# Kernel tuning notes

Hardware: AMD Instinct MI355X
Metric: run time of the kernel (lower is better)

Reference implementation:

```python
import jax, jax.numpy as jnp
import numpy as np

KERNEL_MUL = 2.0
KERNEL_NUM = 5
EPS = 1e-06


def setup_inputs() -> dict:
    key = jax.random.key(0)
    k1, k2 = jax.random.split(key)
    N, D = 4096, 256
    source = jax.random.normal(k1, (N, D), dtype=jnp.float32)
    target = jax.random.normal(k2, (N, D), dtype=jnp.float32)
    return {"source": source, "target": target}


def reference(source, target):
    n_src = source.shape[0]
    total = jnp.concatenate([source, target], axis=0)  # [2N, D]
    n = total.shape[0]
    # the broadcasted (total0 - total1)**2 sum, without the O(N^2*D) tensor).
    sq = jnp.sum(total * total, axis=1)  # [2N]
    L2 = sq[:, None] + sq[None, :] - 2.0 * (total @ total.T)  # [2N, 2N]
    # Bandwidth from detached distances (torch uses L2_distance.data).
    bandwidth = jax.lax.stop_gradient(jnp.sum(L2)) / (n * n - n)
    bandwidth = bandwidth / (KERNEL_MUL ** (KERNEL_NUM // 2))
    kernels = jnp.zeros_like(L2)
    for i in range(KERNEL_NUM):
        bw = bandwidth * (KERNEL_MUL ** i)
        kernels = kernels + jnp.exp(-L2 / (bw + EPS))
    XX = kernels[:n_src, :n_src]
    YY = kernels[n_src:, n_src:]
    XY = kernels[:n_src, n_src:]
    YX = kernels[n_src:, :n_src]
    return jnp.mean(XX + YY - XY - YX)
```

## Files before the change

### kernel.cpp

```cpp
#include <hip/hip_runtime.h>

#define N_TOT 8192
#define NS 4096
#define D 256
#define NB 64
#define NTRI (NB*(NB+1)/2)
#define HALF_B 32

typedef float f32x16 __attribute__((ext_vector_type(16)));
typedef float f32x2 __attribute__((ext_vector_type(2)));
typedef int i32x4 __attribute__((ext_vector_type(4)));
typedef int i32x8 __attribute__((ext_vector_type(8)));

__device__ __forceinline__ void gload16(const void* g, void* l) {
  __builtin_amdgcn_global_load_lds(
      (const __attribute__((address_space(1))) unsigned int*)g,
      (__attribute__((address_space(3))) unsigned int*)l,
      16, 0, 0);
}

__global__ void k_prep(const float* __restrict__ src, const float* __restrict__ tgt,
                       unsigned char* __restrict__ Xb, float* __restrict__ sqv,
                       float* __restrict__ pm, float* __restrict__ wsqp) {
  __shared__ float colacc[256];
  __shared__ float wred[4];
  int t = threadIdx.x, l = t & 63, w = t >> 6;
  colacc[t] = 0.f;
  __syncthreads();
  int base = blockIdx.x * 32;
  float c0 = 0.f, c1 = 0.f, c2 = 0.f, c3 = 0.f;
  float wsq = 0.f;
  #pragma unroll
  for (int r = 0; r < 8; ++r) {
    int row = base + w * 8 + r;
    const float* p = (row < NS) ? (src + (size_t)row * D) : (tgt + (size_t)(row - NS) * D);
    float4 v = ((const float4*)p)[l];
    int pk = __builtin_amdgcn_cvt_pk_fp8_f32(v.x, v.y, 0, false);
    pk = __builtin_amdgcn_cvt_pk_fp8_f32(v.z, v.w, pk, true);
    ((int*)(Xb + (size_t)row * D))[l] = pk;
    c0 += v.x; c1 += v.y; c2 += v.z; c3 += v.w;
    float s = fmaf(v.x, v.x, fmaf(v.y, v.y, fmaf(v.z, v.z, v.w * v.w)));
    for (int o = 32; o > 0; o >>= 1) s += __shfl_down(s, o, 64);
    if (l == 0) { sqv[row] = s; wsq += s; }
  }
  atomicAdd(&colacc[4 * l + 0], c0);
  atomicAdd(&colacc[4 * l + 1], c1);
  atomicAdd(&colacc[4 * l + 2], c2);
  atomicAdd(&colacc[4 * l + 3], c3);
  if (l == 0) wred[w] = wsq;
  __syncthreads();
  pm[blockIdx.x * 256 + t] = colacc[t];
  if (t == 0) wsqp[blockIdx.x] = (wred[0] + wred[1]) + (wred[2] + wred[3]);
}

__global__ void k_bw(const float* __restrict__ pm, const float* __restrict__ wsqp,
                     float* __restrict__ coef) {
  __shared__ double red[256];
  int t = threadIdx.x;
  float cs = 0.f;
  for (int b = 0; b < 256; ++b) cs += pm[b * 256 + t];
  red[t] = (double)cs * (double)cs;
  __syncthreads();
  for (int s = 128; s > 0; s >>= 1) {
    if (t < s) red[t] += red[t + s];
    __syncthreads();
  }
  double msq = red[0];
  __syncthreads();
  red[t] = (double)wsqp[t];
  __syncthreads();
  for (int s = 128; s > 0; s >>= 1) {
    if (t < s) red[t] += red[t + s];
    __syncthreads();
  }
  if (t == 0) {
    double Sv = red[0];
    double n = (double)N_TOT;
    double sumL2 = 2.0 * n * Sv - 2.0 * msq;
    double bw = sumL2 / (n * n - n) / 4.0;
    double c4 = 1.0 / (bw * 16.0 + 1e-6);
    coef[0] = (float)(c4 * 1.4426950408889634);
  }
}

__global__ __launch_bounds__(256) void k_main(
    const unsigned char* __restrict__ Xb, const float* __restrict__ sqv,
    const float* __restrict__ coef, float* __restrict__ bpart) {
  int b = blockIdx.x;
  int bi = (int)((2.f * NB + 1.f - sqrtf((float)((2 * NB + 1) * (2 * NB + 1) - 8 * b))) * 0.5f);
  if (bi < 0) bi = 0;
  if (bi > NB - 1) bi = NB - 1;
  while ((bi + 1) * (2 * NB - bi) / 2 <= b) ++bi;
  while (bi * (2 * NB - bi + 1) / 2 > b) --bi;
  int bj = bi + (b - bi * (2 * NB - bi + 1) / 2);

  __shared__ __align__(16) unsigned char ldsA[4 * 128 * 64];
  __shared__ __align__(16) unsigned char ldsB[4 * 128 * 64];
  __shared__ float sqA[128], sqB[128];
  __shared__ float redw[4];

  int t = threadIdx.x, l = t & 63, w = t >> 6;
  int lr = l & 31, half = l >> 5;
  int waveRow = w >> 1, waveCol = w & 1;

  const unsigned char* arow = Xb + (size_t)bi * 128 * D;
  const unsigned char* brow = Xb + (size_t)bj * 128 * D;

  #pragma unroll
  for (int p = 0; p < 2; ++p) {
    int seg = p * 256 + t;
    int row = seg >> 2;
    int kb = (seg & 3) ^ (row & 3) ^ ((row >> 2) & 3);
    int gbase = row * D + kb * 16;
    int dbase = (p * 256 + w * 64) * 16;
    #pragma unroll
    for (int ko = 0; ko < 4; ++ko) {
      gload16(arow + gbase + ko * 64, &ldsA[ko * 8192 + dbase]);
      gload16(brow + gbase + ko * 64, &ldsB[ko * 8192 + dbase]);
    }
  }
  if (t < 128) sqA[t] = sqv[bi * 128 + t];
  else         sqB[t - 128] = sqv[bj * 128 + (t - 128)];
  float A4 = coef[0];
  __syncthreads();

  f32x16 acc[2][2] = {};
  int cLo = 2 * half, cHi = 2 * half + 1;

  #pragma unroll
  for (int ko = 0; ko < 4; ++ko) {
    const unsigned char* lA = &ldsA[ko * 8192];
    const unsigned char* lB = &ldsB[ko * 8192];
    i32x8 aF[2];
    #pragma unroll
    for (int rb = 0; rb < 2; ++rb) {
      int rowA = waveRow * 64 + rb * 32 + lr;
      int sw = (rowA & 3) ^ ((rowA >> 2) & 3);
      i32x4 lo = *(const i32x4*)&lA[rowA * 64 + (cLo ^ sw) * 16];
      i32x4 hi = *(const i32x4*)&lA[rowA * 64 + (cHi ^ sw) * 16];
      aF[rb] = (i32x8){lo.x, lo.y, lo.z, lo.w, hi.x, hi.y, hi.z, hi.w};
    }
    #pragma unroll
    for (int cb = 0; cb < 2; ++cb) {
      int rowB = waveCol * 64 + cb * 32 + lr;
      int sw = (rowB & 3) ^ ((rowB >> 2) & 3);
      i32x4 lo = *(const i32x4*)&lB[rowB * 64 + (cLo ^ sw) * 16];
      i32x4 hi = *(const i32x4*)&lB[rowB * 64 + (cHi ^ sw) * 16];
      i32x8 bF = (i32x8){lo.x, lo.y, lo.z, lo.w, hi.x, hi.y, hi.z, hi.w};
      #pragma unroll
      for (int rb = 0; rb < 2; ++rb)
        acc[rb][cb] = __builtin_amdgcn_mfma_scale_f32_32x32x64_f8f6f4(
            aF[rb], bF, acc[rb][cb], 0, 0, 0, 127, 0, 127);
    }
  }

  float c2A4 = 2.f * A4, nA4 = -A4;
  f32x2 lsum2 = {0.f, 0.f};
  bool diag = (bi == bj);
  #pragma unroll
  for (int cb = 0; cb < 2; ++cb) {
    int jj = waveCol * 64 + cb * 32 + lr;
    float bjv = nA4 * sqB[jj];
    #pragma unroll
    for (int rb = 0; rb < 2; ++rb) {
      #pragma unroll
      for (int r = 0; r < 16; r += 2) {
        int ii = waveRow * 64 + rb * 32 + (r & 3) + 8 * (r >> 2) + 4 * half;
        f32x2 dot2 = {acc[rb][cb][r], acc[rb][cb][r + 1]};
        f32x2 sq2 = {sqA[ii], sqA[ii + 1]};
        f32x2 tt = c2A4 * dot2 + (nA4 * sq2 + bjv);
        f32x2 e;
        e.x = __builtin_amdgcn_exp2f(tt.x);
        e.y = __builtin_amdgcn_exp2f(tt.y);
        f32x2 e2 = e * e, e4 = e2 * e2, e8 = e4 * e4, e16 = e8 * e8;
        f32x2 kern = ((e + e2) + (e4 + e8)) + e16;
        if (diag) {
          if (ii == jj) kern.x = 0.f;
          if (ii + 1 == jj) kern.y = 0.f;
        }
        lsum2 += kern;
      }
    }
  }
  float lsum = lsum2.x + lsum2.y;
  for (int o = 32; o > 0; o >>= 1) lsum += __shfl_down(lsum, o, 64);
  if (l == 0) redw[w] = lsum;
  __syncthreads();
  if (t == 0) {
    float tot = (redw[0] + redw[1]) + (redw[2] + redw[3]);
    float wgt = diag ? 1.f : 2.f;
    float sgn = ((bi < HALF_B) == (bj < HALF_B)) ? 1.f : -1.f;
    bpart[b] = tot * wgt * sgn;
  }
}

__global__ void k_final(const float* __restrict__ bpart, float* __restrict__ out) {
  __shared__ double red[256];
  int t = threadIdx.x;
  double s = 0.0;
  for (int k = 0; k < 9; ++k) {
    int idx = k * 256 + t;
    if (idx < NTRI) s += (double)bpart[idx];
  }
  red[t] = s;
  __syncthreads();
  for (int st = 128; st > 0; st >>= 1) {
    if (t < st) red[t] += red[t + st];
    __syncthreads();
  }
  if (t == 0) {
    double total = red[0] + 5.0 * (double)N_TOT;
    out[0] = (float)(total / ((double)NS * (double)NS));
  }
}

extern "C" void kernel_launch(void* const* d_in, const int* in_sizes, int n_in,
                              void* d_out, int out_size, void* d_ws, size_t ws_size,
                              hipStream_t stream) {
  const float* src = (const float*)d_in[0];
  const float* tgt = (const float*)d_in[1];
  float* out = (float*)d_out;
  char* ws = (char*)d_ws;
  unsigned char* Xb = (unsigned char*)ws;
  float* sqv  = (float*)(ws + (4u << 20));
  float* pm   = (float*)(ws + (4u << 20) + (32u << 10));
  float* wsqp = (float*)(ws + (4u << 20) + (288u << 10));
  float* coef = (float*)(ws + (4u << 20) + (289u << 10));
  float* bpart = (float*)(ws + (4u << 20) + (290u << 10));

  hipLaunchKernelGGL(k_prep, dim3(256), dim3(256), 0, stream, src, tgt, Xb, sqv, pm, wsqp);
  hipLaunchKernelGGL(k_bw, dim3(1), dim3(256), 0, stream, pm, wsqp, coef);
  hipLaunchKernelGGL(k_main, dim3(NTRI), dim3(256), 0, stream, Xb, sqv, coef, bpart);
  hipLaunchKernelGGL(k_final, dim3(1), dim3(256), 0, stream, bpart, out);
}
```

Baseline: 98.45 us.

## Process two triangle tiles per block with double-buffered K-chunk pipelining

```diff
diff --git a/kernel.cpp b/kernel.cpp
--- a/kernel.cpp
+++ b/kernel.cpp
@@ -86,51 +86,68 @@
 __global__ __launch_bounds__(256) void k_main(
     const unsigned char* __restrict__ Xb, const float* __restrict__ sqv,
     const float* __restrict__ coef, float* __restrict__ bpart) {
-  int b = blockIdx.x;
-  int bi = (int)((2.f * NB + 1.f - sqrtf((float)((2 * NB + 1) * (2 * NB + 1) - 8 * b))) * 0.5f);
-  if (bi < 0) bi = 0;
-  if (bi > NB - 1) bi = NB - 1;
-  while ((bi + 1) * (2 * NB - bi) / 2 <= b) ++bi;
-  while (bi * (2 * NB - bi + 1) / 2 > b) --bi;
-  int bj = bi + (b - bi * (2 * NB - bi + 1) / 2);
-
-  __shared__ __align__(16) unsigned char ldsA[4 * 128 * 64];
-  __shared__ __align__(16) unsigned char ldsB[4 * 128 * 64];
-  __shared__ float sqA[128], sqB[128];
+  int b0 = blockIdx.x * 2;
+  int bi0 = (int)((2.f * NB + 1.f - sqrtf((float)((2 * NB + 1) * (2 * NB + 1) - 8 * b0))) * 0.5f);
+  if (bi0 < 0) bi0 = 0;
+  if (bi0 > NB - 1) bi0 = NB - 1;
+  while ((bi0 + 1) * (2 * NB - bi0) / 2 <= b0) ++bi0;
+  while (bi0 * (2 * NB - bi0 + 1) / 2 > b0) --bi0;
+  int bj0 = bi0 + (b0 - bi0 * (2 * NB - bi0 + 1) / 2);
+  int bi_[2], bj_[2];
+  bi_[0] = bi0; bj_[0] = bj0;
+  bool wrap = (bj0 + 1 > NB - 1);
+  bi_[1] = wrap ? bi0 + 1 : bi0;
+  bj_[1] = wrap ? bi_[1] : bj0 + 1;
+
+  __shared__ __align__(16) unsigned char lds[2][2][8192];
+  __shared__ float sqbuf[2][2][128];
   __shared__ float redw[4];
 
   int t = threadIdx.x, l = t & 63, w = t >> 6;
   int lr = l & 31, half = l >> 5;
   int waveRow = w >> 1, waveCol = w & 1;
 
-  const unsigned char* arow = Xb + (size_t)bi * 128 * D;
-  const unsigned char* brow = Xb + (size_t)bj * 128 * D;
-
-  #pragma unroll
-  for (int p = 0; p < 2; ++p) {
-    int seg = p * 256 + t;
-    int row = seg >> 2;
-    int kb = (seg & 3) ^ (row & 3) ^ ((row >> 2) & 3);
-    int gbase = row * D + kb * 16;
-    int dbase = (p * 256 + w * 64) * 16;
+  float A4 = coef[0];
+  asm volatile("" :: "s"(A4));
+
+  const unsigned char* ar[2] = {Xb + (size_t)bi_[0] * 128 * D, Xb + (size_t)bi_[1] * 128 * D};
+  const unsigned char* br[2] = {Xb + (size_t)bj_[0] * 128 * D, Xb + (size_t)bj_[1] * 128 * D};
+
+  auto STAGE = [&](int s) {
+    int tile = s >> 2, ko = s & 3, c = s & 1;
     #pragma unroll
-    for (int ko = 0; ko < 4; ++ko) {
-      gload16(arow + gbase + ko * 64, &ldsA[ko * 8192 + dbase]);
-      gload16(brow + gbase + ko * 64, &ldsB[ko * 8192 + dbase]);
-    }
-  }
-  if (t < 128) sqA[t] = sqv[bi * 128 + t];
-  else         sqB[t - 128] = sqv[bj * 128 + (t - 128)];
-  float A4 = coef[0];
-  __syncthreads();
+    for (int p = 0; p < 2; ++p) {
+      int seg = p * 256 + t;
+      int row = seg >> 2;
+      int kb = (seg & 3) ^ (row & 3) ^ ((row >> 2) & 3);
+      int goff = row * D + ko * 64 + kb * 16;
+      int dbase = (p * 256 + w * 64) * 16;
+      gload16(ar[tile] + goff, &lds[c][0][dbase]);
+      gload16(br[tile] + goff, &lds[c][1][dbase]);
+    }
+  };
+
+  {
+    int tt2 = t >> 7, rr = t & 127;
+    float sA = sqv[bi_[tt2] * 128 + rr];
+    float sB = sqv[bj_[tt2] * 128 + rr];
+    sqbuf[tt2][0][rr] = sA;
+    sqbuf[tt2][1][rr] = sB;
+  }
+  asm volatile("" ::: "memory");
+  STAGE(0);
+  STAGE(1);
+  asm volatile("s_waitcnt vmcnt(4)" ::: "memory");
+  __builtin_amdgcn_s_barrier();
 
   f32x16 acc[2][2] = {};
   int cLo = 2 * half, cHi = 2 * half + 1;
 
   #pragma unroll
-  for (int ko = 0; ko < 4; ++ko) {
-    const unsigned char* lA = &ldsA[ko * 8192];
-    const unsigned char* lB = &ldsB[ko * 8192];
+  for (int s = 0; s < 8; ++s) {
+    const int tile = s >> 2, cur = s & 1;
+    const unsigned char* lA = &lds[cur][0][0];
+    const unsigned char* lB = &lds[cur][1][0];
     i32x8 aF[2];
     #pragma unroll
     for (int rb = 0; rb < 2; ++rb) {
@@ -152,45 +169,61 @@
         acc[rb][cb] = __builtin_amdgcn_mfma_scale_f32_32x32x64_f8f6f4(
             aF[rb], bF, acc[rb][cb], 0, 0, 0, 127, 0, 127);
     }
-  }
-
-  float c2A4 = 2.f * A4, nA4 = -A4;
-  f32x2 lsum2 = {0.f, 0.f};
-  bool diag = (bi == bj);
-  #pragma unroll
-  for (int cb = 0; cb < 2; ++cb) {
-    int jj = waveCol * 64 + cb * 32 + lr;
-    float bjv = nA4 * sqB[jj];
-    #pragma unroll
-    for (int rb = 0; rb < 2; ++rb) {
+    asm volatile("s_waitcnt lgkmcnt(0)" ::: "memory");
+    __builtin_amdgcn_s_barrier();
+    if (s + 2 < 8) STAGE(s + 2);
+
+    if ((s & 3) == 3) {
+      float c2A4 = 2.f * A4, nA4 = -A4;
+      f32x2 lsum2 = {0.f, 0.f};
+      bool diag = (bi_[tile] == bj_[tile]);
       #pragma unroll
-      for (int r = 0; r < 16; r += 2) {
-        int ii = waveRow * 64 + rb * 32 + (r & 3) + 8 * (r >> 2) + 4 * half;
-        f32x2 dot2 = {acc[rb][cb][r], acc[rb][cb][r + 1]};
-        f32x2 sq2 = {sqA[ii], sqA[ii + 1]};
-        f32x2 tt = c2A4 * dot2 + (nA4 * sq2 + bjv);
-        f32x2 e;
-        e.x = __builtin_amdgcn_exp2f(tt.x);
-        e.y = __builtin_amdgcn_exp2f(tt.y);
-        f32x2 e2 = e * e, e4 = e2 * e2, e8 = e4 * e4, e16 = e8 * e8;
-        f32x2 kern = ((e + e2) + (e4 + e8)) + e16;
-        if (diag) {
-          if (ii == jj) kern.x = 0.f;
-          if (ii + 1 == jj) kern.y = 0.f;
+      for (int cb = 0; cb < 2; ++cb) {
+        int jj = waveCol * 64 + cb * 32 + lr;
+        float bjv = nA4 * sqbuf[tile][1][jj];
+        #pragma unroll
+        for (int rb = 0; rb < 2; ++rb) {
+          #pragma unroll
+          for (int r = 0; r < 16; r += 2) {
+            int ii = waveRow * 64 + rb * 32 + (r & 3) + 8 * (r >> 2) + 4 * half;
+            f32x2 dot2 = {acc[rb][cb][r], acc[rb][cb][r + 1]};
+            f32x2 sq2 = {sqbuf[tile][0][ii], sqbuf[tile][0][ii + 1]};
+            f32x2 tt = c2A4 * dot2 + (nA4 * sq2 + bjv);
+            f32x2 e;
+            e.x = __builtin_amdgcn_exp2f(tt.x);
+            e.y = __builtin_amdgcn_exp2f(tt.y);
+            f32x2 e2 = e * e, e4 = e2 * e2, e8 = e4 * e4, e16 = e8 * e8;
+            f32x2 kern = ((e + e2) + (e4 + e8)) + e16;
+            if (diag) {
+              if (ii == jj) kern.x = 0.f;
+              if (ii + 1 == jj) kern.y = 0.f;
+            }
+            lsum2 += kern;
+          }
         }
-        lsum2 += kern;
       }
-    }
-  }
-  float lsum = lsum2.x + lsum2.y;
-  for (int o = 32; o > 0; o >>= 1) lsum += __shfl_down(lsum, o, 64);
-  if (l == 0) redw[w] = lsum;
-  __syncthreads();
-  if (t == 0) {
-    float tot = (redw[0] + redw[1]) + (redw[2] + redw[3]);
-    float wgt = diag ? 1.f : 2.f;
-    float sgn = ((bi < HALF_B) == (bj < HALF_B)) ? 1.f : -1.f;
-    bpart[b] = tot * wgt * sgn;
+      float lsum = lsum2.x + lsum2.y;
+      for (int o = 32; o > 0; o >>= 1) lsum += __shfl_down(lsum, o, 64);
+      if (l == 0) redw[w] = lsum;
+      asm volatile("s_waitcnt lgkmcnt(0)" ::: "memory");
+      __builtin_amdgcn_s_barrier();
+      if (t == 0) {
+        float tot = (redw[0] + redw[1]) + (redw[2] + redw[3]);
+        float wgt = diag ? 1.f : 2.f;
+        float sgn = ((bi_[tile] < HALF_B) == (bj_[tile] < HALF_B)) ? 1.f : -1.f;
+        bpart[b0 + tile] = tot * wgt * sgn;
+      }
+      #pragma unroll
+      for (int rb2 = 0; rb2 < 2; ++rb2)
+        #pragma unroll
+        for (int cb2 = 0; cb2 < 2; ++cb2)
+          #pragma unroll
+          for (int q = 0; q < 16; ++q) acc[rb2][cb2][q] = 0.f;
+    }
+
+    if (s < 6)       asm volatile("s_waitcnt vmcnt(4)" ::: "memory");
+    else if (s == 6) asm volatile("s_waitcnt vmcnt(0)" ::: "memory");
+    if (s < 7) __builtin_amdgcn_s_barrier();
   }
 }
 
@@ -230,6 +263,6 @@
 
   hipLaunchKernelGGL(k_prep, dim3(256), dim3(256), 0, stream, src, tgt, Xb, sqv, pm, wsqp);
   hipLaunchKernelGGL(k_bw, dim3(1), dim3(256), 0, stream, pm, wsqp, coef);
-  hipLaunchKernelGGL(k_main, dim3(NTRI), dim3(256), 0, stream, Xb, sqv, coef, bpart);
+  hipLaunchKernelGGL(k_main, dim3(NTRI / 2), dim3(256), 0, stream, Xb, sqv, coef, bpart);
   hipLaunchKernelGGL(k_final, dim3(1), dim3(256), 0, stream, bpart, out);
 }
```

After: 98.95 us. About the same (+0.5%).
